# Optimization experiments

Measured on AMD Instinct MI355X. Metric: run time of the kernel, lower is better.

The kernel has to match this reference:

```python
import jax, jax.numpy as jnp
import numpy as np

R = 8
EPS = 1e-08


def diff_x(t, r):
    # t: (B,C,H,W), running cumsum along H -> windowed sum along H
    left = t[:, :, r:2 * r + 1]
    middle = t[:, :, 2 * r + 1:] - t[:, :, :-2 * r - 1]
    right = t[:, :, -1:] - t[:, :, -2 * r - 1:-r - 1]
    return jnp.concatenate([left, middle, right], axis=2)


def diff_y(t, r):
    left = t[:, :, :, r:2 * r + 1]
    middle = t[:, :, :, 2 * r + 1:] - t[:, :, :, :-2 * r - 1]
    right = t[:, :, :, -1:] - t[:, :, :, -2 * r - 1:-r - 1]
    return jnp.concatenate([left, middle, right], axis=3)


def box_filter(x, r):
    return diff_y(diff_x(jnp.cumsum(x, axis=2), r).cumsum(axis=3), r)


def bilinear_align_corners(x, H, W):
    # x: (B,C,h,w) -> (B,C,H,W), matching F.interpolate(mode='bilinear', align_corners=True)
    h, w = x.shape[2], x.shape[3]
    ys = jnp.linspace(0.0, h - 1.0, H, dtype=x.dtype)
    xs = jnp.linspace(0.0, w - 1.0, W, dtype=x.dtype)
    y0 = jnp.clip(jnp.floor(ys).astype(jnp.int32), 0, h - 1)
    x0 = jnp.clip(jnp.floor(xs).astype(jnp.int32), 0, w - 1)
    y1 = jnp.clip(y0 + 1, 0, h - 1)
    x1 = jnp.clip(x0 + 1, 0, w - 1)
    wy = (ys - y0.astype(x.dtype))[:, None]   # (H,1)
    wx = (xs - x0.astype(x.dtype))[None, :]   # (1,W)
    v00 = x[:, :, y0[:, None], x0[None, :]]
    v01 = x[:, :, y0[:, None], x1[None, :]]
    v10 = x[:, :, y1[:, None], x0[None, :]]
    v11 = x[:, :, y1[:, None], x1[None, :]]
    top = v00 * (1 - wx) + v01 * wx
    bot = v10 * (1 - wx) + v11 * wx
    return top * (1 - wy) + bot * wy


def setup_inputs() -> dict:
    key = jax.random.key(0)
    k1, k2, k3 = jax.random.split(key, 3)
    lr_x = jax.random.uniform(k1, (4, 3, 512, 512), dtype=jnp.float32)
    lr_y = jax.random.uniform(k2, (4, 3, 512, 512), dtype=jnp.float32)
    hr_x = jax.random.uniform(k3, (4, 3, 2048, 2048), dtype=jnp.float32)
    return {"lr_x": lr_x, "lr_y": lr_y, "hr_x": hr_x}


def reference(lr_x, lr_y, hr_x):
    _, _, h_lr, w_lr = lr_x.shape
    _, _, h_hr, w_hr = hr_x.shape
    N = box_filter(jnp.ones((1, 1, h_lr, w_lr), dtype=lr_x.dtype), R)
    mean_x = box_filter(lr_x, R) / N
    mean_y = box_filter(lr_y, R) / N
    cov_xy = box_filter(lr_x * lr_y, R) / N - mean_x * mean_y
    var_x = box_filter(lr_x * lr_x, R) / N - mean_x * mean_x
    A = cov_xy / (var_x + EPS)
    b = mean_y - A * mean_x
    mean_A = bilinear_align_corners(A, h_hr, w_hr)
    mean_b = bilinear_align_corners(b, h_hr, w_hr)
    return mean_A * hr_x + mean_b
```

## Files before the change

### kernel.cpp

```cpp
#include <hip/hip_runtime.h>

#define RR 8
#define TILE 32
#define EXT (TILE + 2 * RR)

__global__ __launch_bounds__(256) void k_ab(
    const float* __restrict__ lrx, const float* __restrict__ lry,
    float* __restrict__ Aout, float* __restrict__ Bout, int H, int W) {
  __shared__ float sx[EXT][EXT];
  __shared__ float sy[EXT][EXT];
  __shared__ float hx[EXT][TILE];
  __shared__ float hy[EXT][TILE];
  __shared__ float hxy[EXT][TILE];
  __shared__ float hxx[EXT][TILE];

  const int bc = blockIdx.z;
  const size_t plane = (size_t)bc * H * W;
  const float* __restrict__ px = lrx + plane;
  const float* __restrict__ py = lry + plane;
  const int tx0 = blockIdx.x * TILE;
  const int ty0 = blockIdx.y * TILE;
  const int tid = threadIdx.y * 32 + threadIdx.x;

  for (int i = tid; i < EXT * EXT; i += 256) {
    int r = i / EXT, c = i % EXT;
    int gy = ty0 + r - RR, gx = tx0 + c - RR;
    float vx = 0.f, vy = 0.f;
    if (gy >= 0 && gy < H && gx >= 0 && gx < W) {
      size_t o = (size_t)gy * W + gx;
      vx = px[o];
      vy = py[o];
    }
    sx[r][c] = vx;
    sy[r][c] = vy;
  }
  __syncthreads();

  for (int q = tid; q < EXT * (TILE / 4); q += 256) {
    int r = q >> 3;
    int c0 = (q & 7) * 4;
    float xv[20], yv[20];
#pragma unroll
    for (int t = 0; t < 5; ++t) {
      float4 x4 = *(const float4*)&sx[r][c0 + 4 * t];
      float4 y4 = *(const float4*)&sy[r][c0 + 4 * t];
      xv[4 * t + 0] = x4.x; xv[4 * t + 1] = x4.y; xv[4 * t + 2] = x4.z; xv[4 * t + 3] = x4.w;
      yv[4 * t + 0] = y4.x; yv[4 * t + 1] = y4.y; yv[4 * t + 2] = y4.z; yv[4 * t + 3] = y4.w;
    }
    float pv[20], qv[20];
#pragma unroll
    for (int i = 0; i < 20; ++i) { pv[i] = xv[i] * yv[i]; qv[i] = xv[i] * xv[i]; }
    float ax = 0.f, ay = 0.f, axy = 0.f, axx = 0.f;
#pragma unroll
    for (int i = 0; i < 17; ++i) { ax += xv[i]; ay += yv[i]; axy += pv[i]; axx += qv[i]; }
    float4 ox, oy, oxy, oxx;
    ox.x = ax; oy.x = ay; oxy.x = axy; oxx.x = axx;
#pragma unroll
    for (int j = 1; j < 4; ++j) {
      ax += xv[j + 16] - xv[j - 1];
      ay += yv[j + 16] - yv[j - 1];
      axy += pv[j + 16] - pv[j - 1];
      axx += qv[j + 16] - qv[j - 1];
      (&ox.x)[j] = ax; (&oy.x)[j] = ay; (&oxy.x)[j] = axy; (&oxx.x)[j] = axx;
    }
    *(float4*)&hx[r][c0] = ox;
    *(float4*)&hy[r][c0] = oy;
    *(float4*)&hxy[r][c0] = oxy;
    *(float4*)&hxx[r][c0] = oxx;
  }
  __syncthreads();

  const int c = threadIdx.x;
  const int r0 = threadIdx.y * 4;
  float vx[20], vy[20], vxy[20], vxx[20];
#pragma unroll
  for (int i = 0; i < 20; ++i) {
    vx[i] = hx[r0 + i][c];
    vy[i] = hy[r0 + i][c];
    vxy[i] = hxy[r0 + i][c];
    vxx[i] = hxx[r0 + i][c];
  }
  float sX = 0.f, sY = 0.f, sXY = 0.f, sXX = 0.f;
#pragma unroll
  for (int i = 0; i < 17; ++i) { sX += vx[i]; sY += vy[i]; sXY += vxy[i]; sXX += vxx[i]; }

  const int gx = tx0 + c;
  const int nx = min(gx + RR, W - 1) - max(gx - RR, 0) + 1;
#pragma unroll
  for (int j = 0; j < 4; ++j) {
    if (j > 0) {
      sX += vx[j + 16] - vx[j - 1];
      sY += vy[j + 16] - vy[j - 1];
      sXY += vxy[j + 16] - vxy[j - 1];
      sXX += vxx[j + 16] - vxx[j - 1];
    }
    const int gy = ty0 + r0 + j;
    const int ny = min(gy + RR, H - 1) - max(gy - RR, 0) + 1;
    float inv = 1.f / (float)(nx * ny);
    float mx = sX * inv;
    float my = sY * inv;
    float cov = sXY * inv - mx * my;
    float var = sXX * inv - mx * mx;
    float a = cov / (var + 1e-8f);
    float bv = my - a * mx;
    size_t o = plane + (size_t)gy * W + gx;
    Aout[o] = a;
    Bout[o] = bv;
  }
}

#define KO_LDSW 264
__global__ __launch_bounds__(256) void k_out(
    const float* __restrict__ A, const float* __restrict__ Bb,
    const float* __restrict__ hr, float* __restrict__ out,
    int hl, int wl, int Hh, int Wh) {
  __shared__ float Ay[KO_LDSW];
  __shared__ float By[KO_LDSW];

  const int y = blockIdx.y;
  const int bc = blockIdx.z;
  const int xb = blockIdx.x * 1024;

  const float scy = (float)(hl - 1) / (float)(Hh - 1);
  const float scx = (float)(wl - 1) / (float)(Wh - 1);

  float fy = (float)y * scy;
  int y0 = (int)fy;
  if (y0 > hl - 1) y0 = hl - 1;
  int y1 = y0 + 1;
  if (y1 > hl - 1) y1 = hl - 1;
  const float wy = fy - (float)y0;

  const int x0base = (int)((float)xb * scx);
  int x0max = (int)((float)(xb + 1023) * scx);
  const int nW = x0max - x0base + 2;

  const size_t lrBase = (size_t)bc * hl * wl;
  const float* __restrict__ A0 = A + lrBase + (size_t)y0 * wl;
  const float* __restrict__ A1 = A + lrBase + (size_t)y1 * wl;
  const float* __restrict__ B0 = Bb + lrBase + (size_t)y0 * wl;
  const float* __restrict__ B1 = Bb + lrBase + (size_t)y1 * wl;

  for (int i = threadIdx.x; i < nW; i += 256) {
    int xl = x0base + i;
    if (xl > wl - 1) xl = wl - 1;
    float a0 = A0[xl], a1 = A1[xl];
    float b0 = B0[xl], b1 = B1[xl];
    Ay[i] = a0 + (a1 - a0) * wy;
    By[i] = b0 + (b1 - b0) * wy;
  }
  __syncthreads();

  const int xg = xb + threadIdx.x * 4;
  const size_t hrIdx = ((size_t)bc * Hh + y) * Wh + xg;
  const float4 h4 = *(const float4*)(hr + hrIdx);
  const float hv[4] = {h4.x, h4.y, h4.z, h4.w};
  float res[4];
#pragma unroll
  for (int j = 0; j < 4; ++j) {
    float fx = (float)(xg + j) * scx;
    int x0 = (int)fx;
    float wx = fx - (float)x0;
    int li = x0 - x0base;
    float a = Ay[li] + (Ay[li + 1] - Ay[li]) * wx;
    float b = By[li] + (By[li + 1] - By[li]) * wx;
    res[j] = a * hv[j] + b;
  }
  *(float4*)(out + hrIdx) = make_float4(res[0], res[1], res[2], res[3]);
}

extern "C" void kernel_launch(void* const* d_in, const int* in_sizes, int n_in,
                              void* d_out, int out_size, void* d_ws, size_t ws_size,
                              hipStream_t stream) {
  const float* lrx = (const float*)d_in[0];
  const float* lry = (const float*)d_in[1];
  const float* hrx = (const float*)d_in[2];
  float* out = (float*)d_out;

  const int BC = 12;
  const int hl = 512, wl = 512;
  const int Hh = 2048, Wh = 2048;

  float* A = (float*)d_ws;
  float* B = A + (size_t)BC * hl * wl;

  dim3 g1(wl / TILE, hl / TILE, BC);
  dim3 b1(32, 8);
  k_ab<<<g1, b1, 0, stream>>>(lrx, lry, A, B, hl, wl);

  dim3 g2(Wh / 1024, Hh, BC);
  dim3 b2(256);
  k_out<<<g2, b2, 0, stream>>>(A, B, hrx, out, hl, wl, Hh, Wh);
}
```

Before: 373.0 us.

## Process four output rows per block with shared low-res rows and nontemporal IO

The upsample kernel now handles four consecutive high-res rows per block. It stages three low-res rows of A and B in LDS once and does the full bilinear interpolation per output row, which cuts the number of blocks and the repeated low-res loads. High-res input and output go through nontemporal loads and stores to avoid polluting the cache. The A/B kernel gains a float4 fast path for interior tiles. Risks are higher LDS reads per output and the assumption that four output rows always span at most three low-res rows.

Result: faster. 359.7 us (-3.6%).

```diff
diff --git a/kernel.cpp b/kernel.cpp
--- a/kernel.cpp
+++ b/kernel.cpp
@@ -3,6 +3,8 @@
 #define RR 8
 #define TILE 32
 #define EXT (TILE + 2 * RR)
+
+typedef float f4 __attribute__((ext_vector_type(4)));
 
 __global__ __launch_bounds__(256) void k_ab(
     const float* __restrict__ lrx, const float* __restrict__ lry,
@@ -22,17 +24,30 @@
   const int ty0 = blockIdx.y * TILE;
   const int tid = threadIdx.y * 32 + threadIdx.x;
 
-  for (int i = tid; i < EXT * EXT; i += 256) {
-    int r = i / EXT, c = i % EXT;
-    int gy = ty0 + r - RR, gx = tx0 + c - RR;
-    float vx = 0.f, vy = 0.f;
-    if (gy >= 0 && gy < H && gx >= 0 && gx < W) {
-      size_t o = (size_t)gy * W + gx;
-      vx = px[o];
-      vy = py[o];
-    }
-    sx[r][c] = vx;
-    sy[r][c] = vy;
+  const bool interior = (tx0 >= RR) && (ty0 >= RR) &&
+                        (tx0 + TILE + RR <= W) && (ty0 + TILE + RR <= H);
+  if (interior) {
+    const size_t base = (size_t)(ty0 - RR) * W + (tx0 - RR);
+    for (int i = tid; i < EXT * (EXT / 4); i += 256) {
+      int r = i / (EXT / 4);
+      int c4 = (i - r * (EXT / 4)) * 4;
+      size_t o = base + (size_t)r * W + c4;
+      *(float4*)&sx[r][c4] = *(const float4*)(px + o);
+      *(float4*)&sy[r][c4] = *(const float4*)(py + o);
+    }
+  } else {
+    for (int i = tid; i < EXT * EXT; i += 256) {
+      int r = i / EXT, c = i % EXT;
+      int gy = ty0 + r - RR, gx = tx0 + c - RR;
+      float vx = 0.f, vy = 0.f;
+      if (gy >= 0 && gy < H && gx >= 0 && gx < W) {
+        size_t o = (size_t)gy * W + gx;
+        vx = px[o];
+        vy = py[o];
+      }
+      sx[r][c] = vx;
+      sy[r][c] = vy;
+    }
   }
   __syncthreads();
 
@@ -114,59 +129,97 @@
     const float* __restrict__ A, const float* __restrict__ Bb,
     const float* __restrict__ hr, float* __restrict__ out,
     int hl, int wl, int Hh, int Wh) {
-  __shared__ float Ay[KO_LDSW];
-  __shared__ float By[KO_LDSW];
-
-  const int y = blockIdx.y;
+  __shared__ float As[3][KO_LDSW];
+  __shared__ float Bs[3][KO_LDSW];
+
+  const int yb = blockIdx.y * 4;
   const int bc = blockIdx.z;
   const int xb = blockIdx.x * 1024;
 
   const float scy = (float)(hl - 1) / (float)(Hh - 1);
   const float scx = (float)(wl - 1) / (float)(Wh - 1);
 
-  float fy = (float)y * scy;
-  int y0 = (int)fy;
-  if (y0 > hl - 1) y0 = hl - 1;
-  int y1 = y0 + 1;
-  if (y1 > hl - 1) y1 = hl - 1;
-  const float wy = fy - (float)y0;
+  int v;
+  {
+    float fy0 = (float)yb * scy;
+    int t = (int)fy0;
+    if (t > hl - 1) t = hl - 1;
+    v = t;
+  }
+
+  int ry0[4], ry1[4];
+  float wyv[4];
+#pragma unroll
+  for (int r = 0; r < 4; ++r) {
+    float fy = (float)(yb + r) * scy;
+    int y0 = (int)fy;
+    if (y0 > hl - 1) y0 = hl - 1;
+    int y1 = y0 + 1;
+    if (y1 > hl - 1) y1 = hl - 1;
+    wyv[r] = fy - (float)y0;
+    ry0[r] = y0 - v;
+    ry1[r] = y1 - v;
+  }
 
   const int x0base = (int)((float)xb * scx);
-  int x0max = (int)((float)(xb + 1023) * scx);
-  const int nW = x0max - x0base + 2;
-
   const size_t lrBase = (size_t)bc * hl * wl;
-  const float* __restrict__ A0 = A + lrBase + (size_t)y0 * wl;
-  const float* __restrict__ A1 = A + lrBase + (size_t)y1 * wl;
-  const float* __restrict__ B0 = Bb + lrBase + (size_t)y0 * wl;
-  const float* __restrict__ B1 = Bb + lrBase + (size_t)y1 * wl;
-
-  for (int i = threadIdx.x; i < nW; i += 256) {
-    int xl = x0base + i;
+
+  for (int i = threadIdx.x; i < 3 * KO_LDSW; i += 256) {
+    int rr = i / KO_LDSW;
+    int cc = i - rr * KO_LDSW;
+    int xl = x0base + cc;
     if (xl > wl - 1) xl = wl - 1;
-    float a0 = A0[xl], a1 = A1[xl];
-    float b0 = B0[xl], b1 = B1[xl];
-    Ay[i] = a0 + (a1 - a0) * wy;
-    By[i] = b0 + (b1 - b0) * wy;
+    int yr = v + rr;
+    if (yr > hl - 1) yr = hl - 1;
+    size_t o = lrBase + (size_t)yr * wl + xl;
+    As[rr][cc] = A[o];
+    Bs[rr][cc] = Bb[o];
   }
   __syncthreads();
 
   const int xg = xb + threadIdx.x * 4;
-  const size_t hrIdx = ((size_t)bc * Hh + y) * Wh + xg;
-  const float4 h4 = *(const float4*)(hr + hrIdx);
-  const float hv[4] = {h4.x, h4.y, h4.z, h4.w};
-  float res[4];
+  int li[4];
+  float wxv[4];
 #pragma unroll
   for (int j = 0; j < 4; ++j) {
     float fx = (float)(xg + j) * scx;
     int x0 = (int)fx;
-    float wx = fx - (float)x0;
-    int li = x0 - x0base;
-    float a = Ay[li] + (Ay[li + 1] - Ay[li]) * wx;
-    float b = By[li] + (By[li + 1] - By[li]) * wx;
-    res[j] = a * hv[j] + b;
-  }
-  *(float4*)(out + hrIdx) = make_float4(res[0], res[1], res[2], res[3]);
+    wxv[j] = fx - (float)x0;
+    li[j] = x0 - x0base;
+  }
+
+  const size_t hrBase = ((size_t)bc * Hh + yb) * Wh + xg;
+  f4 h[4];
+#pragma unroll
+  for (int r = 0; r < 4; ++r)
+    h[r] = __builtin_nontemporal_load((const f4*)(hr + hrBase + (size_t)r * Wh));
+
+#pragma unroll
+  for (int r = 0; r < 4; ++r) {
+    const float* __restrict__ a0 = As[ry0[r]];
+    const float* __restrict__ a1 = As[ry1[r]];
+    const float* __restrict__ b0 = Bs[ry0[r]];
+    const float* __restrict__ b1 = Bs[ry1[r]];
+    const float wy = wyv[r];
+    f4 res;
+#pragma unroll
+    for (int j = 0; j < 4; ++j) {
+      int l = li[j];
+      float w = wxv[j];
+      float a00 = a0[l], a01 = a0[l + 1];
+      float a10 = a1[l], a11 = a1[l + 1];
+      float c00 = b0[l], c01 = b0[l + 1];
+      float c10 = b1[l], c11 = b1[l + 1];
+      float at = a00 + (a01 - a00) * w;
+      float ab = a10 + (a11 - a10) * w;
+      float bt = c00 + (c01 - c00) * w;
+      float bbv = c10 + (c11 - c10) * w;
+      float a = at + (ab - at) * wy;
+      float b = bt + (bbv - bt) * wy;
+      res[j] = a * h[r][j] + b;
+    }
+    __builtin_nontemporal_store(res, (f4*)(out + hrBase + (size_t)r * Wh));
+  }
 }
 
 extern "C" void kernel_launch(void* const* d_in, const int* in_sizes, int n_in,
@@ -188,7 +241,7 @@
   dim3 b1(32, 8);
   k_ab<<<g1, b1, 0, stream>>>(lrx, lry, A, B, hl, wl);
 
-  dim3 g2(Wh / 1024, Hh, BC);
+  dim3 g2(Wh / 1024, Hh / 4, BC);
   dim3 b2(256);
   k_out<<<g2, b2, 0, stream>>>(A, B, hrx, out, hl, wl, Hh, Wh);
 }
```

## Vectorize interior tile loads and process full output rows per block with nontemporal IO

Applied to the files above, without the earlier changes.

In k_ab, interior tiles now load the haloed input patch with float4 global loads, and only edge tiles keep the scalar bounds-checked loop. In k_out, each block now covers a whole 2048-wide output row, staging the full 512-wide vertically interpolated A/B row in LDS with float2 loads. Each thread handles two float4 chunks using nontemporal loads and stores, and the hr loads are issued before the barrier to overlap with staging. This halves the block count and avoids cache pollution from streaming data, at the cost of hardcoded width assumptions (512/2048) in the staging code.

Measured after the change: 369.4 us. Within noise of the previous version (-1.0%).

```diff
diff --git a/kernel.cpp b/kernel.cpp
--- a/kernel.cpp
+++ b/kernel.cpp
@@ -3,6 +3,8 @@
 #define RR 8
 #define TILE 32
 #define EXT (TILE + 2 * RR)
+
+typedef float f4 __attribute__((ext_vector_type(4)));
 
 __global__ __launch_bounds__(256) void k_ab(
     const float* __restrict__ lrx, const float* __restrict__ lry,
@@ -22,17 +24,30 @@
   const int ty0 = blockIdx.y * TILE;
   const int tid = threadIdx.y * 32 + threadIdx.x;
 
-  for (int i = tid; i < EXT * EXT; i += 256) {
-    int r = i / EXT, c = i % EXT;
-    int gy = ty0 + r - RR, gx = tx0 + c - RR;
-    float vx = 0.f, vy = 0.f;
-    if (gy >= 0 && gy < H && gx >= 0 && gx < W) {
-      size_t o = (size_t)gy * W + gx;
-      vx = px[o];
-      vy = py[o];
-    }
-    sx[r][c] = vx;
-    sy[r][c] = vy;
+  const bool interior = (tx0 >= RR) && (ty0 >= RR) &&
+                        (tx0 + TILE + RR <= W) && (ty0 + TILE + RR <= H);
+  if (interior) {
+    const size_t base = (size_t)(ty0 - RR) * W + (tx0 - RR);
+    for (int i = tid; i < EXT * (EXT / 4); i += 256) {
+      int r = i / (EXT / 4);
+      int c4 = (i - r * (EXT / 4)) * 4;
+      size_t o = base + (size_t)r * W + c4;
+      *(float4*)&sx[r][c4] = *(const float4*)(px + o);
+      *(float4*)&sy[r][c4] = *(const float4*)(py + o);
+    }
+  } else {
+    for (int i = tid; i < EXT * EXT; i += 256) {
+      int r = i / EXT, c = i % EXT;
+      int gy = ty0 + r - RR, gx = tx0 + c - RR;
+      float vx = 0.f, vy = 0.f;
+      if (gy >= 0 && gy < H && gx >= 0 && gx < W) {
+        size_t o = (size_t)gy * W + gx;
+        vx = px[o];
+        vy = py[o];
+      }
+      sx[r][c] = vx;
+      sy[r][c] = vy;
+    }
   }
   __syncthreads();
 
@@ -109,17 +124,17 @@
   }
 }
 
-#define KO_LDSW 264
+#define KO_W 514
 __global__ __launch_bounds__(256) void k_out(
     const float* __restrict__ A, const float* __restrict__ Bb,
     const float* __restrict__ hr, float* __restrict__ out,
     int hl, int wl, int Hh, int Wh) {
-  __shared__ float Ay[KO_LDSW];
-  __shared__ float By[KO_LDSW];
-
-  const int y = blockIdx.y;
-  const int bc = blockIdx.z;
-  const int xb = blockIdx.x * 1024;
+  __shared__ float Ay[KO_W];
+  __shared__ float By[KO_W];
+
+  const int y = blockIdx.x;
+  const int bc = blockIdx.y;
+  const int tid = threadIdx.x;
 
   const float scy = (float)(hl - 1) / (float)(Hh - 1);
   const float scx = (float)(wl - 1) / (float)(Wh - 1);
@@ -131,42 +146,59 @@
   if (y1 > hl - 1) y1 = hl - 1;
   const float wy = fy - (float)y0;
 
-  const int x0base = (int)((float)xb * scx);
-  int x0max = (int)((float)(xb + 1023) * scx);
-  const int nW = x0max - x0base + 2;
-
   const size_t lrBase = (size_t)bc * hl * wl;
   const float* __restrict__ A0 = A + lrBase + (size_t)y0 * wl;
   const float* __restrict__ A1 = A + lrBase + (size_t)y1 * wl;
   const float* __restrict__ B0 = Bb + lrBase + (size_t)y0 * wl;
   const float* __restrict__ B1 = Bb + lrBase + (size_t)y1 * wl;
 
-  for (int i = threadIdx.x; i < nW; i += 256) {
-    int xl = x0base + i;
-    if (xl > wl - 1) xl = wl - 1;
-    float a0 = A0[xl], a1 = A1[xl];
-    float b0 = B0[xl], b1 = B1[xl];
-    Ay[i] = a0 + (a1 - a0) * wy;
-    By[i] = b0 + (b1 - b0) * wy;
-  }
+  {
+    const int c2 = 2 * tid;
+    float2 a0 = *(const float2*)(A0 + c2);
+    float2 a1 = *(const float2*)(A1 + c2);
+    float2 b0 = *(const float2*)(B0 + c2);
+    float2 b1 = *(const float2*)(B1 + c2);
+    float ay0 = a0.x + (a1.x - a0.x) * wy;
+    float ay1 = a0.y + (a1.y - a0.y) * wy;
+    float by0 = b0.x + (b1.x - b0.x) * wy;
+    float by1 = b0.y + (b1.y - b0.y) * wy;
+    *(float2*)&Ay[c2] = make_float2(ay0, ay1);
+    *(float2*)&By[c2] = make_float2(by0, by1);
+    if (tid == 255) {
+      Ay[512] = ay1;
+      By[512] = by1;
+    }
+  }
+
+  const size_t rowBase = ((size_t)bc * Hh + y) * Wh;
+  const int xg0 = tid * 4;
+  const int xg1 = 1024 + tid * 4;
+  f4 h0 = __builtin_nontemporal_load((const f4*)(hr + rowBase + xg0));
+  f4 h1 = __builtin_nontemporal_load((const f4*)(hr + rowBase + xg1));
+
   __syncthreads();
 
-  const int xg = xb + threadIdx.x * 4;
-  const size_t hrIdx = ((size_t)bc * Hh + y) * Wh + xg;
-  const float4 h4 = *(const float4*)(hr + hrIdx);
-  const float hv[4] = {h4.x, h4.y, h4.z, h4.w};
-  float res[4];
+  f4 res0, res1;
 #pragma unroll
   for (int j = 0; j < 4; ++j) {
-    float fx = (float)(xg + j) * scx;
+    float fx = (float)(xg0 + j) * scx;
     int x0 = (int)fx;
     float wx = fx - (float)x0;
-    int li = x0 - x0base;
-    float a = Ay[li] + (Ay[li + 1] - Ay[li]) * wx;
-    float b = By[li] + (By[li + 1] - By[li]) * wx;
-    res[j] = a * hv[j] + b;
-  }
-  *(float4*)(out + hrIdx) = make_float4(res[0], res[1], res[2], res[3]);
+    float a = Ay[x0] + (Ay[x0 + 1] - Ay[x0]) * wx;
+    float b = By[x0] + (By[x0 + 1] - By[x0]) * wx;
+    res0[j] = a * h0[j] + b;
+  }
+#pragma unroll
+  for (int j = 0; j < 4; ++j) {
+    float fx = (float)(xg1 + j) * scx;
+    int x0 = (int)fx;
+    float wx = fx - (float)x0;
+    float a = Ay[x0] + (Ay[x0 + 1] - Ay[x0]) * wx;
+    float b = By[x0] + (By[x0 + 1] - By[x0]) * wx;
+    res1[j] = a * h1[j] + b;
+  }
+  __builtin_nontemporal_store(res0, (f4*)(out + rowBase + xg0));
+  __builtin_nontemporal_store(res1, (f4*)(out + rowBase + xg1));
 }
 
 extern "C" void kernel_launch(void* const* d_in, const int* in_sizes, int n_in,
@@ -188,7 +220,7 @@
   dim3 b1(32, 8);
   k_ab<<<g1, b1, 0, stream>>>(lrx, lry, A, B, hl, wl);
 
-  dim3 g2(Wh / 1024, Hh, BC);
+  dim3 g2(Hh, BC);
   dim3 b2(256);
   k_out<<<g2, b2, 0, stream>>>(A, B, hrx, out, hl, wl, Hh, Wh);
 }
```
